# Performance work log

Hardware: AMD Instinct MI355X
Metric: run time of the kernel (lower is better)

## Reference

```python
import jax, jax.numpy as jnp
import numpy as np

CH = 64          # channels
OC = 64          # out_channels
B, H, W = 8, 128, 128
NCA_C = CH + OC  # 128, NCA state channels
K = 3            # kernel_size
DILS = (1, 2, 4, 8)
HID = 64         # NCA update hidden
EPS = 1e-5


def setup_inputs() -> dict:
    key = jax.random.key(0)
    ks = jax.random.split(key, 16)
    def n(k, shape, s=0.02):
        return jax.random.normal(k, shape, jnp.float32) * s
    return {
        "x": jax.random.normal(ks[0], (B, H, W, CH), jnp.float32),
        "c": jax.random.normal(ks[1], (B, OC), jnp.float32),
        # Attention params
        "Wq": n(ks[2], (CH, OC)), "bq": jnp.zeros((OC,), jnp.float32),
        "Wk": n(ks[3], (OC, OC)), "bk": jnp.zeros((OC,), jnp.float32),
        "Wv": n(ks[4], (OC, OC)), "bv": jnp.zeros((OC,), jnp.float32),
        "Wo": n(ks[5], (OC, OC)), "bo": jnp.zeros((OC,), jnp.float32),
        "ln_g": jnp.ones((OC,), jnp.float32), "ln_b": jnp.zeros((OC,), jnp.float32),
        # NCA depthwise perception kernels, one per dilation: [4, NCA_C, 1, K, K]
        "pk": n(ks[6], (len(DILS), NCA_C, 1, K, K), 0.1),
        # NCA update MLP
        "W1": n(ks[7], ((1 + len(DILS)) * NCA_C, HID)), "b1": jnp.zeros((HID,), jnp.float32),
        "W2": n(ks[8], (HID, CH)), "b2": jnp.zeros((CH,), jnp.float32),
    }


def _layernorm(z, g, b):
    m = jnp.mean(z, axis=-1, keepdims=True)
    v = jnp.var(z, axis=-1, keepdims=True)
    return (z - m) / jnp.sqrt(v + EPS) * g + b


def _forward(x, c, Wq, bq, Wk, bk, Wv, bv, Wo, bo, ln_g, ln_b, pk, W1, b1, W2, b2):
    b_, h_, w_, _ = x.shape
    # ---- Attention(x, c): single-key softmax pooling over H*W ----
    q = x.reshape(b_, h_ * w_, CH) @ Wq + bq              # [B, HW, OC]
    k = c @ Wk + bk                                        # [B, OC]
    v = c @ Wv + bv                                        # [B, OC]
    scores = jnp.einsum('bno,bo->bn', q, k) * (OC ** -0.5)  # [B, HW]
    attn = jax.nn.softmax(scores, axis=1)                  # softmax over spatial dim
    attended = jnp.einsum('bn,bo->bo', attn, v)            # weighted pool (weights sum to 1)
    a = _layernorm(attended @ Wo + bo + c, ln_g, ln_b)     # out_proj + residual + LN
    c2 = c + a                                             # outer residual in NCAAttention

    # ---- concat broadcast context -> NCA state [B,H,W,NCA_C] ----
    c_exp = jnp.broadcast_to(c2[:, None, None, :], (b_, h_, w_, OC))
    xc = jnp.concatenate([x, c_exp], axis=-1)

    # ---- NCA perception: depthwise dilated convs (SAME padding) ----
    xp = jnp.transpose(xc, (0, 3, 1, 2))                   # NCHW
    feats = [xc]
    for i, d in enumerate(DILS):
        pad = d * (K // 2)
        p = jax.lax.conv_general_dilated(
            xp, pk[i], window_strides=(1, 1),
            padding=[(pad, pad), (pad, pad)], rhs_dilation=(d, d),
            dimension_numbers=('NCHW', 'OIHW', 'NCHW'),
            feature_group_count=NCA_C)
        feats.append(jnp.transpose(p, (0, 2, 3, 1)))
    upd_in = jnp.concatenate(feats, axis=-1)               # [B,H,W,5*NCA_C]

    # ---- NCA update MLP: Linear -> (Dropout=id) -> GELU -> Linear ----
    hidden = jax.nn.gelu(upd_in @ W1 + b1, approximate=False)
    y = hidden @ W2 + b2                                   # [B,H,W,CH]
    # NCA.out_channels (64) != NCA.channels (128) -> no residual add
    return y, c2


def reference(x, c, Wq, bq, Wk, bk, Wv, bv, Wo, bo, ln_g, ln_b, pk, W1, b1, W2, b2):
    return _forward(x, c, Wq, bq, Wk, bk, Wv, bv, Wo, bo, ln_g, ln_b, pk, W1, b1, W2, b2)
```

## Files before the change

kernel.cpp:

```cpp
#include <hip/hip_runtime.h>
#include <hip/hip_bf16.h>
#include <math.h>


typedef float  f32x4 __attribute__((ext_vector_type(4)));
typedef short  s16x8 __attribute__((ext_vector_type(8)));
typedef long   i64x2 __attribute__((ext_vector_type(2)));

static __device__ __forceinline__ unsigned short f2bf(float f) {
    __hip_bfloat16 h = __float2bfloat16(f);
    unsigned short u; __builtin_memcpy(&u, &h, 2); return u;
}
static __device__ __forceinline__ unsigned pk4fp8(float f0, float f1, float f2, float f3) {
    int v = 0;
    v = __builtin_amdgcn_cvt_pk_fp8_f32(f0, f1, v, false);
    v = __builtin_amdgcn_cvt_pk_fp8_f32(f2, f3, v, true);
    return (unsigned)v;
}

#define XROWB  9216
#define XBATCH 1327104
#define USCALE 256.0f

__global__ void prep1(const float* __restrict__ c,
                      const float* __restrict__ Wv, const float* __restrict__ bv,
                      const float* __restrict__ Wo, const float* __restrict__ bo,
                      const float* __restrict__ lng, const float* __restrict__ lnb,
                      float* __restrict__ c2f, float* __restrict__ outc2)
{
    const int b = blockIdx.x, j = threadIdx.x;
    __shared__ float sc[64], sv[64];
    float cj = c[b*64 + j];
    sc[j] = cj; __syncthreads();
    float v = bv[j];
    for (int i = 0; i < 64; ++i) v += sc[i]*Wv[i*64 + j];
    sv[j] = v; __syncthreads();
    float t = bo[j] + cj;
    for (int i = 0; i < 64; ++i) t += sv[i]*Wo[i*64 + j];
    float s = t;
    for (int o = 32; o > 0; o >>= 1) s += __shfl_xor(s, o);
    float m = s * (1.f/64.f);
    float dq = (t - m)*(t - m);
    for (int o = 32; o > 0; o >>= 1) dq += __shfl_xor(dq, o);
    float a = (t - m) / sqrtf(dq*(1.f/64.f) + 1e-5f) * lng[j] + lnb[j];
    float c2 = cj + a;
    c2f[b*64 + j] = c2;
    outc2[b*64 + j] = c2;
}

__global__ void prep2(const float* __restrict__ x,  const float* __restrict__ pk,
                      const float* __restrict__ W1, const float* __restrict__ W2,
                      const float* __restrict__ b1, const float* __restrict__ c2f,
                      unsigned char* __restrict__ xp, unsigned char* __restrict__ Uf,
                      unsigned short* __restrict__ W2s,
                      float* __restrict__ V, float* __restrict__ hcp)
{
    const int blk = blockIdx.x, tid = threadIdx.x;
    if (blk < 512) {
        int i = blk*256 + tid;
        int xc = i & 127, y = (i >> 7) & 127, b = i >> 14;
        const float* src = x + (size_t)i*64;
        float4 f[16];
        #pragma unroll
        for (int k = 0; k < 16; ++k) f[k] = *(const float4*)(src + k*4);
        unsigned P[16];
        #pragma unroll
        for (int k = 0; k < 16; ++k) P[k] = pk4fp8(f[k].x, f[k].y, f[k].z, f[k].w);
        unsigned char* d = xp + (size_t)b*XBATCH + (size_t)(y+8)*XROWB + (size_t)(xc+8)*64;
        *(uint4*)(d +  0) = make_uint4(P[0], P[1], P[8],  P[9]);
        *(uint4*)(d + 16) = make_uint4(P[2], P[3], P[10], P[11]);
        *(uint4*)(d + 32) = make_uint4(P[4], P[5], P[12], P[13]);
        *(uint4*)(d + 48) = make_uint4(P[6], P[7], P[14], P[15]);
    } else if (blk < 648) {
        int idx = (blk - 512)*256 + tid;
        int b = idx / 4352, r = idx - b*4352;
        int yy, xx;
        if (r < 2304) { int ry = r / 144; xx = r - ry*144; yy = (ry < 8) ? ry : 128 + ry; }
        else { int r2 = r - 2304; yy = 8 + (r2 >> 4); int xi = r2 & 15; xx = (xi < 8) ? xi : 128 + xi; }
        unsigned char* d = xp + (size_t)b*XBATCH + (size_t)yy*XROWB + (size_t)xx*64;
        uint4 z = make_uint4(0,0,0,0);
        *(uint4*)(d) = z; *(uint4*)(d+16) = z; *(uint4*)(d+32) = z; *(uint4*)(d+48) = z;
    } else if (blk < 681) {
        int idx = (blk - 648)*256 + tid;
        if (idx < 8448) {
            int lane = idx & 63, nt = (idx >> 6) & 3, pos = idx >> 8;
            int n  = nt*16 + (lane & 15);
            static constexpr int DI[33] = {3,3,3, 2,2,2, 1,1,1, 0,0,0, -1, 0,0, 1,1, 2,2, 3,3,
                                           0,0,0, 1,1,1, 2,2,2, 3,3,3};
            static constexpr int TT[33] = {0,1,2, 0,1,2, 0,1,2, 0,1,2, 4, 3,5, 3,5, 3,5, 3,5,
                                           6,7,8, 6,7,8, 6,7,8, 6,7,8};
            int di = DI[pos], t = TT[pos];
            float vv[16];
            #pragma unroll
            for (int kc2 = 0; kc2 < 2; ++kc2)
                #pragma unroll
                for (int j = 0; j < 8; ++j) {
                    int ch = kc2*32 + (lane >> 4)*8 + j;
                    float v;
                    if (di < 0) {
                        v = W1[ch*64 + n];
                        for (int dd = 0; dd < 4; ++dd)
                            v += pk[(dd*128 + ch)*9 + 4] * W1[((1+dd)*128 + ch)*64 + n];
                    } else {
                        v = pk[(di*128 + ch)*9 + t] * W1[((1+di)*128 + ch)*64 + n];
                    }
                    vv[kc2*8 + j] = v * USCALE;
                }
            uint4 o;
            o.x = pk4fp8(vv[0],  vv[1],  vv[2],  vv[3]);
            o.y = pk4fp8(vv[4],  vv[5],  vv[6],  vv[7]);
            o.z = pk4fp8(vv[8],  vv[9],  vv[10], vv[11]);
            o.w = pk4fp8(vv[12], vv[13], vv[14], vv[15]);
            *(uint4*)(Uf + (size_t)idx*16) = o;
        }
    } else if (blk < 683) {
        int idx = (blk - 681)*256 + tid;
        int lane = idx & 63, nt = (idx >> 6) & 3, kc2 = (idx >> 8) & 1;
        int n  = nt*16 + (lane & 15);
        int k0 = kc2*32 + (lane >> 4)*8;
        unsigned short e[8];
        #pragma unroll
        for (int j = 0; j < 8; ++j) e[j] = f2bf(W2[(k0+j)*64 + n]);
        uint4 o;
        o.x = (unsigned)e[0] | ((unsigned)e[1] << 16);
        o.y = (unsigned)e[2] | ((unsigned)e[3] << 16);
        o.z = (unsigned)e[4] | ((unsigned)e[5] << 16);
        o.w = (unsigned)e[6] | ((unsigned)e[7] << 16);
        *(uint4*)(W2s + (size_t)idx*8) = o;
    } else if (blk < 755) {
        int idx = (blk - 683)*256 + tid;
        int n = idx & 63, q = idx >> 6;
        int p = q % 36, b = q / 36;
        int di = p/9, t = p%9;
        float s = 0.f;
        for (int j = 0; j < 64; ++j)
            s += c2f[b*64 + j] * pk[(di*128 + 64 + j)*9 + t] * W1[((1+di)*128 + 64 + j)*64 + n];
        V[(size_t)q*64 + n] = s;
    } else {
        for (int it = tid; it < 512; it += 256) {
            int b = it >> 6, n = it & 63;
            float s = b1[n];
            for (int j = 0; j < 64; ++j) s += c2f[b*64 + j]*W1[(64 + j)*64 + n];
            hcp[it] = s;
        }
    }
}

#define HID_S 72

__global__ __launch_bounds__(256) void nca_main(
    const unsigned char* __restrict__ xp,
    const unsigned char* __restrict__ U,
    const unsigned short* __restrict__ W2s,
    const float* __restrict__ V,
    const float* __restrict__ hcp,
    const float* __restrict__ b2,
    float* __restrict__ out)
{
    __shared__ unsigned short hid[256*HID_S];
    __shared__ float V_l[36*64];
    __shared__ float Cx_l[16*64];
    __shared__ float Cy_l[2*64];
    __shared__ float hc2_l[64];

    const int tid = threadIdx.x;
    const int blk = blockIdx.x;
    const int b  = blk & 7;
    const int y0 = (blk >> 3) * 2;

    {
        const float4* Vg = (const float4*)(V + (size_t)b*2304);
        for (int i = tid; i < 576; i += 256) ((float4*)V_l)[i] = Vg[i];
    }
    __syncthreads();
    for (int it = tid; it < 1024; it += 256) {
        int xi = it >> 6, n = it & 63;
        int xx = xi < 8 ? xi : 112 + xi;
        float s = 0.f;
        #pragma unroll
        for (int di = 0; di < 4; ++di) {
            int d = 1 << di;
            int dxo = (xx < d) ? 0 : ((xx >= 128 - d) ? 2 : -1);
            if (dxo >= 0) {
                s += V_l[(di*9 + 0*3 + dxo)*64 + n];
                s += V_l[(di*9 + 1*3 + dxo)*64 + n];
                s += V_l[(di*9 + 2*3 + dxo)*64 + n];
            }
        }
        Cx_l[it] = s;
    }
    for (int it = tid; it < 128; it += 256) {
        int r = it >> 6, n = it & 63;
        int yy = y0 + r;
        float s = 0.f;
        #pragma unroll
        for (int di = 0; di < 4; ++di) {
            int d = 1 << di;
            int dyo = (yy < d) ? 0 : ((yy >= 128 - d) ? 2 : -1);
            if (dyo >= 0) {
                s += V_l[(di*9 + dyo*3 + 0)*64 + n];
                s += V_l[(di*9 + dyo*3 + 1)*64 + n];
                s += V_l[(di*9 + dyo*3 + 2)*64 + n];
            }
        }
        Cy_l[it] = s;
    }
    if (tid < 64) {
        float s = hcp[b*64 + tid];
        for (int p = 0; p < 36; ++p) s += V_l[p*64 + tid];
        hc2_l[tid] = s;
    }
    __syncthreads();

    const int lane = tid & 63;
    const int w    = tid >> 6;
    const int y    = y0 + (w >> 1);
    const int xw   = (w & 1) * 64;
    const int ln15 = lane & 15;
    const int oct  = lane >> 4;

    const unsigned char* abase = xp + (size_t)b*XBATCH + (size_t)(y + 8)*XROWB
                               + (size_t)(xw + ln15 + 8)*64 + oct*16;
    const unsigned char* ubase = U + (size_t)lane*16;

    f32x4 acc[4][4];
    #pragma unroll
    for (int mt = 0; mt < 4; ++mt)
        #pragma unroll
        for (int nt = 0; nt < 4; ++nt) {
            acc[mt][nt][0] = 0.f; acc[mt][nt][1] = 0.f;
            acc[mt][nt][2] = 0.f; acc[mt][nt][3] = 0.f;
        }

    static constexpr int OFF[33] = {
        (-8*144-8)*64, (-8*144)*64, (-8*144+8)*64,
        (-4*144-4)*64, (-4*144)*64, (-4*144+4)*64,
        (-2*144-2)*64, (-2*144)*64, (-2*144+2)*64,
        (-1*144-1)*64, (-1*144)*64, (-1*144+1)*64,
        0,
        -64, 64, -128, 128, -256, 256, -512, 512,
        ( 1*144-1)*64, ( 1*144)*64, ( 1*144+1)*64,
        ( 2*144-2)*64, ( 2*144)*64, ( 2*144+2)*64,
        ( 4*144-4)*64, ( 4*144)*64, ( 4*144+4)*64,
        ( 8*144-8)*64, ( 8*144)*64, ( 8*144+8)*64
    };

    i64x2 Ac[4], An[4], Bc[4], Bn[4];
    #pragma unroll
    for (int mt = 0; mt < 4; ++mt) Ac[mt] = *(const i64x2*)(abase + OFF[0] + mt*1024);
    #pragma unroll
    for (int nt = 0; nt < 4; ++nt) Bc[nt] = *(const i64x2*)(ubase + nt*1024);

    #pragma unroll 1
    for (int pos = 0; pos < 33; ++pos) {
        if (pos < 32) {
            const unsigned char* rp = abase + OFF[pos + 1];
            #pragma unroll
            for (int mt = 0; mt < 4; ++mt) An[mt] = *(const i64x2*)(rp + mt*1024);
            const unsigned char* up = ubase + (size_t)(pos + 1)*4096;
            #pragma unroll
            for (int nt = 0; nt < 4; ++nt) Bn[nt] = *(const i64x2*)(up + nt*1024);
        }
        #pragma unroll
        for (int kc2 = 0; kc2 < 2; ++kc2) {
            #pragma unroll
            for (int nt = 0; nt < 4; ++nt) {
                long bf = Bc[nt][kc2];
                #pragma unroll
                for (int mt = 0; mt < 4; ++mt)
                    acc[mt][nt] = __builtin_amdgcn_mfma_f32_16x16x32_fp8_fp8(Ac[mt][kc2], bf, acc[mt][nt], 0, 0, 0);
            }
        }
        #pragma unroll
        for (int mt = 0; mt < 4; ++mt) Ac[mt] = An[mt];
        #pragma unroll
        for (int nt = 0; nt < 4; ++nt) Bc[nt] = Bn[nt];
    }

    const bool yedge = (y < 8) || (y >= 120);
    #pragma unroll
    for (int mt = 0; mt < 4; ++mt) {
        #pragma unroll
        for (int nt = 0; nt < 4; ++nt) {
            const int n = nt*16 + ln15;
            const float hcv = hc2_l[n];
            const float cyv = yedge ? Cy_l[(w >> 1)*64 + n] : 0.f;
            #pragma unroll
            for (int r = 0; r < 4; ++r) {
                int m = oct*4 + r;
                int x = xw + mt*16 + m;
                float h = acc[mt][nt][r]*(1.0f/USCALE) + hcv - cyv;
                if (x < 8 || x >= 120) {
                    int xi = (x < 8) ? x : (x - 112);
                    h -= Cx_l[xi*64 + n];
                    if (yedge) {
                        #pragma unroll
                        for (int di = 0; di < 4; ++di) {
                            int d = 1 << di;
                            int dyo = (y < d) ? 0 : ((y >= 128 - d) ? 2 : -1);
                            int dxo = (x < d) ? 0 : ((x >= 128 - d) ? 2 : -1);
                            if (dyo >= 0 && dxo >= 0)
                                h += V_l[(di*9 + dyo*3 + dxo)*64 + n];
                        }
                    }
                }
                float u = 0.7978845608028654f * (h + 0.044715f*h*h*h);
                float g = h / (1.f + __expf(-2.f*u));
                hid[(w*64 + mt*16 + m)*HID_S + n] = f2bf(g);
            }
        }
    }

    f32x4 acc2[4][4];
    #pragma unroll
    for (int mt = 0; mt < 4; ++mt)
        #pragma unroll
        for (int nt = 0; nt < 4; ++nt) {
            acc2[mt][nt][0] = 0.f; acc2[mt][nt][1] = 0.f;
            acc2[mt][nt][2] = 0.f; acc2[mt][nt][3] = 0.f;
        }
    #pragma unroll
    for (int kc2 = 0; kc2 < 2; ++kc2) {
        s16x8 a2[4];
        #pragma unroll
        for (int mt = 0; mt < 4; ++mt)
            a2[mt] = *(const s16x8*)&hid[(w*64 + mt*16 + ln15)*HID_S + kc2*32 + oct*8];
        #pragma unroll
        for (int nt = 0; nt < 4; ++nt) {
            s16x8 bf = *(const s16x8*)(W2s + ((size_t)(kc2*4 + nt)*64 + lane)*8);
            #pragma unroll
            for (int mt = 0; mt < 4; ++mt)
                acc2[mt][nt] = __builtin_amdgcn_mfma_f32_16x16x32_bf16(a2[mt], bf, acc2[mt][nt], 0, 0, 0);
        }
    }

    float* ob = out + ((size_t)(b*128 + y))*128*64;
    #pragma unroll
    for (int nt = 0; nt < 4; ++nt) {
        const float b2v = b2[nt*16 + ln15];
        #pragma unroll
        for (int mt = 0; mt < 4; ++mt) {
            #pragma unroll
            for (int r = 0; r < 4; ++r) {
                int x = xw + mt*16 + oct*4 + r;
                ob[(size_t)x*64 + nt*16 + ln15] = acc2[mt][nt][r] + b2v;
            }
        }
    }
}

extern "C" void kernel_launch(void* const* d_in, const int* in_sizes, int n_in,
                              void* d_out, int out_size, void* d_ws, size_t ws_size,
                              hipStream_t stream) {
    const float* x   = (const float*)d_in[0];
    const float* c   = (const float*)d_in[1];
    const float* Wv  = (const float*)d_in[6];
    const float* bv  = (const float*)d_in[7];
    const float* Wo  = (const float*)d_in[8];
    const float* bo  = (const float*)d_in[9];
    const float* lng = (const float*)d_in[10];
    const float* lnb = (const float*)d_in[11];
    const float* pk  = (const float*)d_in[12];
    const float* W1  = (const float*)d_in[13];
    const float* b1  = (const float*)d_in[14];
    const float* W2  = (const float*)d_in[15];
    const float* b2  = (const float*)d_in[16];
    float* out = (float*)d_out;

    char* w = (char*)d_ws;
    unsigned char*  xpb = (unsigned char*)(w);
    unsigned char*  Uf  = (unsigned char*)(w + 10616832);
    unsigned short* W2s = (unsigned short*)(w + 10752000);
    float*          V   = (float*)         (w + 10760192);
    float*          hcp = (float*)         (w + 10833920);
    float*          c2f = (float*)         (w + 10835968);

    prep1<<<8, 64, 0, stream>>>(c, Wv, bv, Wo, bo, lng, lnb, c2f, out + 8388608);
    prep2<<<757, 256, 0, stream>>>(x, pk, W1, W2, b1, c2f, xpb, Uf, W2s, V, hcp);
    nca_main<<<512, 256, 0, stream>>>(xpb, Uf, W2s, V, hcp, b2, out);
}
```

Measured before the change: 162.6 us.

## Split NCA main kernel into smaller blocks and precompute edge corrections in prep

Moves the per-block constant corrections (hidden bias plus perception of the broadcast channels, row and column edge terms) out of nca_main into extra prep2 blocks that write them to global memory. nca_main now uses 128-thread blocks covering one 64-pixel row segment, with each wave owning two of the four N tiles, and the grid grows to 2048 blocks. The first GEMM loop becomes a two-stage ping-pong register double buffer. This drops the shared-memory prologue and two barriers in exchange for duplicated A-operand loads across waves, more global reads in the epilogue, and a barrier before the second GEMM.

```diff
diff --git a/kernel.cpp b/kernel.cpp
--- a/kernel.cpp
+++ b/kernel.cpp
@@ -52,8 +52,9 @@
                       const float* __restrict__ W1, const float* __restrict__ W2,
                       const float* __restrict__ b1, const float* __restrict__ c2f,
                       unsigned char* __restrict__ xp, unsigned char* __restrict__ Uf,
-                      unsigned short* __restrict__ W2s,
-                      float* __restrict__ V, float* __restrict__ hcp)
+                      unsigned short* __restrict__ W2s, float* __restrict__ V,
+                      float* __restrict__ hc2g, float* __restrict__ CyG,
+                      float* __restrict__ CxG)
 {
     const int blk = blockIdx.x, tid = threadIdx.x;
     if (blk < 512) {
@@ -136,100 +137,98 @@
         for (int j = 0; j < 64; ++j)
             s += c2f[b*64 + j] * pk[(di*128 + 64 + j)*9 + t] * W1[((1+di)*128 + 64 + j)*64 + n];
         V[(size_t)q*64 + n] = s;
+    } else if (blk < 757) {
+        int idx = (blk - 755)*256 + tid;
+        if (idx < 512) {
+            int b = idx >> 6, n = idx & 63;
+            float s = b1[n];
+            for (int j = 0; j < 64; ++j) {
+                float wsum = W1[(64 + j)*64 + n];
+                for (int di = 0; di < 4; ++di) {
+                    float ks = 0.f;
+                    for (int t = 0; t < 9; ++t) ks += pk[(di*128 + 64 + j)*9 + t];
+                    wsum += ks * W1[((1+di)*128 + 64 + j)*64 + n];
+                }
+                s += c2f[b*64 + j] * wsum;
+            }
+            hc2g[idx] = s;
+        }
+    } else if (blk < 1013) {
+        int idx = (blk - 757)*256 + tid;
+        int n = idx & 63, y = (idx >> 6) & 127, b = idx >> 13;
+        float s = 0.f;
+        for (int di = 0; di < 4; ++di) {
+            int d = 1 << di;
+            int dyo = (y < d) ? 0 : ((y >= 128 - d) ? 2 : -1);
+            if (dyo >= 0) {
+                for (int j = 0; j < 64; ++j) {
+                    float pks = pk[(di*128 + 64 + j)*9 + dyo*3 + 0]
+                              + pk[(di*128 + 64 + j)*9 + dyo*3 + 1]
+                              + pk[(di*128 + 64 + j)*9 + dyo*3 + 2];
+                    s += c2f[b*64 + j] * pks * W1[((1+di)*128 + 64 + j)*64 + n];
+                }
+            }
+        }
+        CyG[idx] = s;
     } else {
-        for (int it = tid; it < 512; it += 256) {
-            int b = it >> 6, n = it & 63;
-            float s = b1[n];
-            for (int j = 0; j < 64; ++j) s += c2f[b*64 + j]*W1[(64 + j)*64 + n];
-            hcp[it] = s;
-        }
+        int idx = (blk - 1013)*256 + tid;
+        int n = idx & 63, xi = (idx >> 6) & 15, b = idx >> 10;
+        int xx = (xi < 8) ? xi : 112 + xi;
+        float s = 0.f;
+        for (int di = 0; di < 4; ++di) {
+            int d = 1 << di;
+            int dxo = (xx < d) ? 0 : ((xx >= 128 - d) ? 2 : -1);
+            if (dxo >= 0) {
+                for (int j = 0; j < 64; ++j) {
+                    float pks = pk[(di*128 + 64 + j)*9 + 0*3 + dxo]
+                              + pk[(di*128 + 64 + j)*9 + 1*3 + dxo]
+                              + pk[(di*128 + 64 + j)*9 + 2*3 + dxo];
+                    s += c2f[b*64 + j] * pks * W1[((1+di)*128 + 64 + j)*64 + n];
+                }
+            }
+        }
+        CxG[idx] = s;
     }
 }
 
 #define HID_S 72
 
-__global__ __launch_bounds__(256) void nca_main(
+__global__ __launch_bounds__(128, 4) void nca_main(
     const unsigned char* __restrict__ xp,
     const unsigned char* __restrict__ U,
     const unsigned short* __restrict__ W2s,
     const float* __restrict__ V,
-    const float* __restrict__ hcp,
+    const float* __restrict__ hc2g,
+    const float* __restrict__ CyG,
+    const float* __restrict__ CxG,
     const float* __restrict__ b2,
     float* __restrict__ out)
 {
-    __shared__ unsigned short hid[256*HID_S];
-    __shared__ float V_l[36*64];
-    __shared__ float Cx_l[16*64];
-    __shared__ float Cy_l[2*64];
-    __shared__ float hc2_l[64];
+    __shared__ unsigned short hid[64*HID_S];
 
     const int tid = threadIdx.x;
     const int blk = blockIdx.x;
     const int b  = blk & 7;
-    const int y0 = (blk >> 3) * 2;
-
-    {
-        const float4* Vg = (const float4*)(V + (size_t)b*2304);
-        for (int i = tid; i < 576; i += 256) ((float4*)V_l)[i] = Vg[i];
-    }
-    __syncthreads();
-    for (int it = tid; it < 1024; it += 256) {
-        int xi = it >> 6, n = it & 63;
-        int xx = xi < 8 ? xi : 112 + xi;
-        float s = 0.f;
-        #pragma unroll
-        for (int di = 0; di < 4; ++di) {
-            int d = 1 << di;
-            int dxo = (xx < d) ? 0 : ((xx >= 128 - d) ? 2 : -1);
-            if (dxo >= 0) {
-                s += V_l[(di*9 + 0*3 + dxo)*64 + n];
-                s += V_l[(di*9 + 1*3 + dxo)*64 + n];
-                s += V_l[(di*9 + 2*3 + dxo)*64 + n];
-            }
-        }
-        Cx_l[it] = s;
-    }
-    for (int it = tid; it < 128; it += 256) {
-        int r = it >> 6, n = it & 63;
-        int yy = y0 + r;
-        float s = 0.f;
-        #pragma unroll
-        for (int di = 0; di < 4; ++di) {
-            int d = 1 << di;
-            int dyo = (yy < d) ? 0 : ((yy >= 128 - d) ? 2 : -1);
-            if (dyo >= 0) {
-                s += V_l[(di*9 + dyo*3 + 0)*64 + n];
-                s += V_l[(di*9 + dyo*3 + 1)*64 + n];
-                s += V_l[(di*9 + dyo*3 + 2)*64 + n];
-            }
-        }
-        Cy_l[it] = s;
-    }
-    if (tid < 64) {
-        float s = hcp[b*64 + tid];
-        for (int p = 0; p < 36; ++p) s += V_l[p*64 + tid];
-        hc2_l[tid] = s;
-    }
-    __syncthreads();
+    const int q  = blk >> 3;
+    const int y  = q >> 1;
+    const int xw = (q & 1) * 64;
 
     const int lane = tid & 63;
     const int w    = tid >> 6;
-    const int y    = y0 + (w >> 1);
-    const int xw   = (w & 1) * 64;
     const int ln15 = lane & 15;
     const int oct  = lane >> 4;
 
     const unsigned char* abase = xp + (size_t)b*XBATCH + (size_t)(y + 8)*XROWB
                                + (size_t)(xw + ln15 + 8)*64 + oct*16;
-    const unsigned char* ubase = U + (size_t)lane*16;
-
-    f32x4 acc[4][4];
+    const unsigned char* ubase = U + (size_t)w*2048 + (size_t)lane*16;
+
+    f32x4 acc[4][2];
     #pragma unroll
     for (int mt = 0; mt < 4; ++mt)
         #pragma unroll
-        for (int nt = 0; nt < 4; ++nt) {
-            acc[mt][nt][0] = 0.f; acc[mt][nt][1] = 0.f;
-            acc[mt][nt][2] = 0.f; acc[mt][nt][3] = 0.f;
+        for (int j = 0; j < 2; ++j) {
+            acc[mt][j][0] = 0.f; acc[mt][j][1] = 0.f;
+            acc[mt][j][2] = 0.f; acc[mt][j][3] = 0.f;
         }
 
     static constexpr int OFF[33] = {
@@ -245,54 +244,58 @@
         ( 8*144-8)*64, ( 8*144)*64, ( 8*144+8)*64
     };
 
-    i64x2 Ac[4], An[4], Bc[4], Bn[4];
-    #pragma unroll
-    for (int mt = 0; mt < 4; ++mt) Ac[mt] = *(const i64x2*)(abase + OFF[0] + mt*1024);
-    #pragma unroll
-    for (int nt = 0; nt < 4; ++nt) Bc[nt] = *(const i64x2*)(ubase + nt*1024);
-
-    #pragma unroll 1
-    for (int pos = 0; pos < 33; ++pos) {
-        if (pos < 32) {
-            const unsigned char* rp = abase + OFF[pos + 1];
-            #pragma unroll
-            for (int mt = 0; mt < 4; ++mt) An[mt] = *(const i64x2*)(rp + mt*1024);
-            const unsigned char* up = ubase + (size_t)(pos + 1)*4096;
-            #pragma unroll
-            for (int nt = 0; nt < 4; ++nt) Bn[nt] = *(const i64x2*)(up + nt*1024);
-        }
-        #pragma unroll
-        for (int kc2 = 0; kc2 < 2; ++kc2) {
-            #pragma unroll
-            for (int nt = 0; nt < 4; ++nt) {
-                long bf = Bc[nt][kc2];
+    i64x2 A0[4], A1[4], B0[2], B1[2];
+    auto loadA = [&](i64x2* A, int pos) {
+        const unsigned char* rp = abase + OFF[pos];
+        #pragma unroll
+        for (int mt = 0; mt < 4; ++mt) A[mt] = *(const i64x2*)(rp + mt*1024);
+    };
+    auto loadB = [&](i64x2* Bv, int pos) {
+        const unsigned char* up = ubase + (size_t)pos*4096;
+        Bv[0] = *(const i64x2*)(up);
+        Bv[1] = *(const i64x2*)(up + 1024);
+    };
+    auto mfblk = [&](i64x2* A, i64x2* Bv) {
+        #pragma unroll
+        for (int kc2 = 0; kc2 < 2; ++kc2)
+            #pragma unroll
+            for (int j = 0; j < 2; ++j) {
+                long bf = Bv[j][kc2];
                 #pragma unroll
                 for (int mt = 0; mt < 4; ++mt)
-                    acc[mt][nt] = __builtin_amdgcn_mfma_f32_16x16x32_fp8_fp8(Ac[mt][kc2], bf, acc[mt][nt], 0, 0, 0);
-            }
-        }
-        #pragma unroll
-        for (int mt = 0; mt < 4; ++mt) Ac[mt] = An[mt];
-        #pragma unroll
-        for (int nt = 0; nt < 4; ++nt) Bc[nt] = Bn[nt];
-    }
+                    acc[mt][j] = __builtin_amdgcn_mfma_f32_16x16x32_fp8_fp8(A[mt][kc2], bf, acc[mt][j], 0, 0, 0);
+            }
+    };
+
+    loadA(A0, 0);  loadB(B0, 0);
+    loadA(A1, 1);  loadB(B1, 1);
+
+    #pragma unroll 1
+    for (int i = 0; i < 16; ++i) {
+        mfblk(A0, B0);
+        int pa = 2*i + 2;
+        loadA(A0, pa); loadB(B0, pa);
+        mfblk(A1, B1);
+        int pb = (2*i + 3 <= 32) ? (2*i + 3) : 32;
+        loadA(A1, pb); loadB(B1, pb);
+    }
+    mfblk(A0, B0);
 
     const bool yedge = (y < 8) || (y >= 120);
     #pragma unroll
-    for (int mt = 0; mt < 4; ++mt) {
-        #pragma unroll
-        for (int nt = 0; nt < 4; ++nt) {
-            const int n = nt*16 + ln15;
-            const float hcv = hc2_l[n];
-            const float cyv = yedge ? Cy_l[(w >> 1)*64 + n] : 0.f;
+    for (int j = 0; j < 2; ++j) {
+        const int n = (w*2 + j)*16 + ln15;
+        const float h0 = hc2g[b*64 + n] - CyG[((b << 7) + y)*64 + n];
+        #pragma unroll
+        for (int mt = 0; mt < 4; ++mt) {
             #pragma unroll
             for (int r = 0; r < 4; ++r) {
-                int m = oct*4 + r;
-                int x = xw + mt*16 + m;
-                float h = acc[mt][nt][r]*(1.0f/USCALE) + hcv - cyv;
+                int m = mt*16 + oct*4 + r;
+                int x = xw + m;
+                float h = acc[mt][j][r]*(1.0f/USCALE) + h0;
                 if (x < 8 || x >= 120) {
                     int xi = (x < 8) ? x : (x - 112);
-                    h -= Cx_l[xi*64 + n];
+                    h -= CxG[((b << 4) + xi)*64 + n];
                     if (yedge) {
                         #pragma unroll
                         for (int di = 0; di < 4; ++di) {
@@ -300,50 +303,53 @@
                             int dyo = (y < d) ? 0 : ((y >= 128 - d) ? 2 : -1);
                             int dxo = (x < d) ? 0 : ((x >= 128 - d) ? 2 : -1);
                             if (dyo >= 0 && dxo >= 0)
-                                h += V_l[(di*9 + dyo*3 + dxo)*64 + n];
+                                h += V[((size_t)b*36 + di*9 + dyo*3 + dxo)*64 + n];
                         }
                     }
                 }
                 float u = 0.7978845608028654f * (h + 0.044715f*h*h*h);
                 float g = h / (1.f + __expf(-2.f*u));
-                hid[(w*64 + mt*16 + m)*HID_S + n] = f2bf(g);
-            }
-        }
-    }
-
-    f32x4 acc2[4][4];
+                hid[m*HID_S + n] = f2bf(g);
+            }
+        }
+    }
+    __syncthreads();
+
+    f32x4 acc2[4][2];
     #pragma unroll
     for (int mt = 0; mt < 4; ++mt)
         #pragma unroll
-        for (int nt = 0; nt < 4; ++nt) {
-            acc2[mt][nt][0] = 0.f; acc2[mt][nt][1] = 0.f;
-            acc2[mt][nt][2] = 0.f; acc2[mt][nt][3] = 0.f;
+        for (int j = 0; j < 2; ++j) {
+            acc2[mt][j][0] = 0.f; acc2[mt][j][1] = 0.f;
+            acc2[mt][j][2] = 0.f; acc2[mt][j][3] = 0.f;
         }
     #pragma unroll
     for (int kc2 = 0; kc2 < 2; ++kc2) {
         s16x8 a2[4];
         #pragma unroll
         for (int mt = 0; mt < 4; ++mt)
-            a2[mt] = *(const s16x8*)&hid[(w*64 + mt*16 + ln15)*HID_S + kc2*32 + oct*8];
-        #pragma unroll
-        for (int nt = 0; nt < 4; ++nt) {
+            a2[mt] = *(const s16x8*)&hid[(mt*16 + ln15)*HID_S + kc2*32 + oct*8];
+        #pragma unroll
+        for (int j = 0; j < 2; ++j) {
+            int nt = w*2 + j;
             s16x8 bf = *(const s16x8*)(W2s + ((size_t)(kc2*4 + nt)*64 + lane)*8);
             #pragma unroll
             for (int mt = 0; mt < 4; ++mt)
-                acc2[mt][nt] = __builtin_amdgcn_mfma_f32_16x16x32_bf16(a2[mt], bf, acc2[mt][nt], 0, 0, 0);
+                acc2[mt][j] = __builtin_amdgcn_mfma_f32_16x16x32_bf16(a2[mt], bf, acc2[mt][j], 0, 0, 0);
         }
     }
 
     float* ob = out + ((size_t)(b*128 + y))*128*64;
     #pragma unroll
-    for (int nt = 0; nt < 4; ++nt) {
-        const float b2v = b2[nt*16 + ln15];
+    for (int j = 0; j < 2; ++j) {
+        const int n = (w*2 + j)*16 + ln15;
+        const float b2v = b2[n];
         #pragma unroll
         for (int mt = 0; mt < 4; ++mt) {
             #pragma unroll
             for (int r = 0; r < 4; ++r) {
                 int x = xw + mt*16 + oct*4 + r;
-                ob[(size_t)x*64 + nt*16 + ln15] = acc2[mt][nt][r] + b2v;
+                ob[(size_t)x*64 + n] = acc2[mt][j][r] + b2v;
             }
         }
     }
@@ -368,14 +374,16 @@
     float* out = (float*)d_out;
 
     char* w = (char*)d_ws;
-    unsigned char*  xpb = (unsigned char*)(w);
-    unsigned char*  Uf  = (unsigned char*)(w + 10616832);
-    unsigned short* W2s = (unsigned short*)(w + 10752000);
-    float*          V   = (float*)         (w + 10760192);
-    float*          hcp = (float*)         (w + 10833920);
-    float*          c2f = (float*)         (w + 10835968);
+    unsigned char*  xpb  = (unsigned char*)(w);
+    unsigned char*  Uf   = (unsigned char*)(w + 10616832);
+    unsigned short* W2s  = (unsigned short*)(w + 10752000);
+    float*          V    = (float*)         (w + 10760192);
+    float*          hc2g = (float*)         (w + 10833920);
+    float*          c2f  = (float*)         (w + 10835968);
+    float*          CyG  = (float*)         (w + 10838016);
+    float*          CxG  = (float*)         (w + 11100160);
 
     prep1<<<8, 64, 0, stream>>>(c, Wv, bv, Wo, bo, lng, lnb, c2f, out + 8388608);
-    prep2<<<757, 256, 0, stream>>>(x, pk, W1, W2, b1, c2f, xpb, Uf, W2s, V, hcp);
-    nca_main<<<512, 256, 0, stream>>>(xpb, Uf, W2s, V, hcp, b2, out);
-}
+    prep2<<<1045, 256, 0, stream>>>(x, pk, W1, W2, b1, c2f, xpb, Uf, W2s, V, hc2g, CyG, CxG);
+    nca_main<<<2048, 128, 0, stream>>>(xpb, Uf, W2s, V, hc2g, CyG, CxG, b2, out);
+}
```

Result: slower. 182.2 us (+12.1%).
